# Performance work log

Hardware: AMD Instinct MI355X
Metric: run time of the kernel (lower is better)

The kernel has to match this reference:

```python
import jax, jax.numpy as jnp
import numpy as np

NUM_HEADS = 8

def setup_inputs() -> dict:
    key = jax.random.key(0)
    k1, k2, k3, k4, k5 = jax.random.split(key, 5)
    B, N, C = 4, 2048, 512
    x = jax.random.normal(k1, (B, N, C), dtype=jnp.float32)
    s = 1.0 / np.sqrt(C)
    qkv_w = jax.random.uniform(k2, (3 * C, C), dtype=jnp.float32, minval=-s, maxval=s)
    qkv_b = jax.random.uniform(k3, (3 * C,), dtype=jnp.float32, minval=-s, maxval=s)
    proj_w = jax.random.uniform(k4, (C, C), dtype=jnp.float32, minval=-s, maxval=s)
    proj_b = jax.random.uniform(k5, (C,), dtype=jnp.float32, minval=-s, maxval=s)
    return {"x": x, "qkv_w": qkv_w, "qkv_b": qkv_b, "proj_w": proj_w, "proj_b": proj_b}

def reference(x, qkv_w, qkv_b, proj_w, proj_b):
    B, N, C = x.shape
    H = NUM_HEADS
    D = C // H
    scale = D ** -0.5
    # qkv: [B,N,3C] -> [3,B,H,N,D]
    qkv = (jnp.einsum('bnc,oc->bno', x, qkv_w) + qkv_b)
    qkv = qkv.reshape(B, N, 3, H, D).transpose(2, 0, 3, 1, 4)
    q, k, v = qkv[0], qkv[1], qkv[2]
    attn = jnp.einsum('bhnd,bhmd->bhnm', q, k) * scale  # [B,H,N,N]
    attn = jax.nn.softmax(attn, axis=-1)
    out = jnp.einsum('bhnm,bhmd->bhnd', attn, v)  # [B,H,N,D]
    out = out.transpose(0, 2, 1, 3).reshape(B, N, C)
    return jnp.einsum('bnc,oc->bno', out, proj_w) + proj_b
```

## Files before the change

### kernel.cpp

```cpp
#include <hip/hip_runtime.h>
#include <stdint.h>


typedef short bf16x8 __attribute__((ext_vector_type(8)));
typedef float f32x2  __attribute__((ext_vector_type(2)));
typedef float f32x4  __attribute__((ext_vector_type(4)));
typedef float f32x16 __attribute__((ext_vector_type(16)));
typedef unsigned int u32x4 __attribute__((ext_vector_type(4)));

__device__ __forceinline__ unsigned short f2bf(float f) {
    unsigned int u = __builtin_bit_cast(unsigned int, f);
    u += 0x7fffu + ((u >> 16) & 1u);
    return (unsigned short)(u >> 16);
}
__device__ __forceinline__ unsigned int pk2(float a, float b) {
    return (unsigned int)f2bf(a) | ((unsigned int)f2bf(b) << 16);
}
__device__ __forceinline__ float fexp2(float x) {
    return __builtin_amdgcn_exp2f(x);
}
__device__ __forceinline__ bf16x8 ld8_f32(const float* __restrict__ p) {
    float4 f0 = *(const float4*)p;
    float4 f1 = *(const float4*)(p + 4);
    u32x4 u = {pk2(f0.x, f0.y), pk2(f0.z, f0.w), pk2(f1.x, f1.y), pk2(f1.z, f1.w)};
    return __builtin_bit_cast(bf16x8, u);
}
__device__ __forceinline__ void async16(const void* g, void* l) {
    __builtin_amdgcn_global_load_lds(
        (const __attribute__((address_space(1))) unsigned int*)g,
        (__attribute__((address_space(3))) unsigned int*)l,
        16, 0, 0);
}

#define MFMA16(a, b, c) __builtin_amdgcn_mfma_f32_16x16x32_bf16((a), (b), (c), 0, 0, 0)
#define MFMA32(a, b, c) __builtin_amdgcn_mfma_f32_32x32x16_bf16((a), (b), (c), 0, 0, 0)

__global__ void cvt_bf16(const float* __restrict__ x,
                         const float* __restrict__ w,
                         unsigned short* __restrict__ xb,
                         unsigned short* __restrict__ wb)
{
    const int G = 524288 + 98304;
    for (int idx = blockIdx.x * 256 + threadIdx.x; idx < G; idx += gridDim.x * 256) {
        if (idx < 524288)
            *(bf16x8*)(xb + (size_t)idx * 8) = ld8_f32(x + (size_t)idx * 8);
        else {
            int j = idx - 524288;
            *(bf16x8*)(wb + (size_t)j * 8) = ld8_f32(w + (size_t)j * 8);
        }
    }
}
__global__ void cvt_w2(const float* __restrict__ w, unsigned short* __restrict__ wb)
{
    int idx = blockIdx.x * 256 + threadIdx.x;
    *(bf16x8*)(wb + (size_t)idx * 8) = ld8_f32(w + (size_t)idx * 8);
}

__global__ __launch_bounds__(256, 4)
void gemm_qkv(const unsigned short* __restrict__ A,
              const unsigned short* __restrict__ B,
              const float* __restrict__ bias,
              unsigned short* __restrict__ out0,
              unsigned short* __restrict__ out1,
              unsigned short* __restrict__ out2,
              int K)
{
    __shared__ unsigned short sA[128 * 32];
    __shared__ unsigned short sB[128 * 32];

    const int tid  = threadIdx.x;
    const int wave = tid >> 6, lane = tid & 63;
    const int l = lane & 15, q16 = lane >> 4;
    const int wm = wave >> 1, wn = wave & 1;
    const int bid = blockIdx.x;
    const int slot = bid >> 3;
    const int m0 = ((bid & 7) * 8 + slot / 12) * 128;
    const int n0 = (slot % 12) * 128;

    f32x4 acc[4][4];
#pragma unroll
    for (int i = 0; i < 4; ++i)
#pragma unroll
        for (int j = 0; j < 4; ++j)
            acc[i][j] = (f32x4){0.f, 0.f, 0.f, 0.f};

    for (int k0 = 0; k0 < K; k0 += 32) {
#pragma unroll
        for (int call = 0; call < 2; ++call) {
            int L = call * 256 + tid;
            int r = L >> 2, c = L & 3;
            async16(A + (size_t)(m0 + r) * K + k0 + c * 8, sA + L * 8);
            async16(B + (size_t)(n0 + r) * K + k0 + c * 8, sB + L * 8);
        }
        __syncthreads();

        bf16x8 af[4], bfr[4];
#pragma unroll
        for (int i = 0; i < 4; ++i)
            af[i] = *(const bf16x8*)(sA + ((wm * 64 + i * 16 + l) * 4 + q16) * 8);
#pragma unroll
        for (int j = 0; j < 4; ++j)
            bfr[j] = *(const bf16x8*)(sB + ((wn * 64 + j * 16 + l) * 4 + q16) * 8);
#pragma unroll
        for (int i = 0; i < 4; ++i)
#pragma unroll
            for (int j = 0; j < 4; ++j)
                acc[i][j] = MFMA16(af[i], bfr[j], acc[i][j]);
        __syncthreads();
    }

    const float lscale = 0.18033688f;
#pragma unroll
    for (int i = 0; i < 4; ++i) {
#pragma unroll
        for (int j = 0; j < 4; ++j) {
            int col = n0 + wn * 64 + j * 16 + l;
            float bv = bias[col];
#pragma unroll
            for (int r = 0; r < 4; ++r) {
                int row = m0 + wm * 64 + i * 16 + q16 * 4 + r;
                float val = acc[i][j][r] + bv;
                int which = col >> 9;
                int h = (col >> 6) & 7, d = col & 63;
                int b = row >> 11, n = row & 2047;
                if (which == 0)
                    out0[(size_t)(((b * 8 + h) * 2048) + n) * 64 + d] = f2bf(val * lscale);
                else if (which == 1)
                    out1[(size_t)(((b * 8 + h) * 2048) + n) * 64 + d] = f2bf(val);
                else {
                    int np = (n & ~12) | ((n & 8) >> 1) | ((n & 4) << 1);
                    out2[(size_t)(((b * 8 + h) * 64) + d) * 2048 + np] = f2bf(val);
                }
            }
        }
    }
}

__global__ __launch_bounds__(256, 4)
void gemm_out(const unsigned short* __restrict__ A,
              const unsigned short* __restrict__ B,
              const float* __restrict__ bias,
              float* __restrict__ outf,
              int K, int N)
{
    __shared__ unsigned short sA[64 * 32];
    __shared__ unsigned short sB[128 * 32];

    const int tid  = threadIdx.x;
    const int wave = tid >> 6, lane = tid & 63;
    const int l = lane & 15, q16 = lane >> 4;
    const int wm = wave >> 1, wn = wave & 1;
    const int bid = blockIdx.x;
    const int slot = bid >> 3;
    const int m0 = ((bid & 7) * 16 + (slot >> 2)) * 64;
    const int n0 = (slot & 3) * 128;

    f32x4 acc[2][4];
#pragma unroll
    for (int i = 0; i < 2; ++i)
#pragma unroll
        for (int j = 0; j < 4; ++j)
            acc[i][j] = (f32x4){0.f, 0.f, 0.f, 0.f};

    for (int k0 = 0; k0 < K; k0 += 32) {
        {
            int r = tid >> 2, c = tid & 3;
            async16(A + (size_t)(m0 + r) * K + k0 + c * 8, sA + tid * 8);
        }
#pragma unroll
        for (int call = 0; call < 2; ++call) {
            int L = call * 256 + tid;
            int r = L >> 2, c = L & 3;
            async16(B + (size_t)(n0 + r) * K + k0 + c * 8, sB + L * 8);
        }
        __syncthreads();

        bf16x8 af[2], bfr[4];
#pragma unroll
        for (int i = 0; i < 2; ++i)
            af[i] = *(const bf16x8*)(sA + ((wm * 32 + i * 16 + l) * 4 + q16) * 8);
#pragma unroll
        for (int j = 0; j < 4; ++j)
            bfr[j] = *(const bf16x8*)(sB + ((wn * 64 + j * 16 + l) * 4 + q16) * 8);
#pragma unroll
        for (int i = 0; i < 2; ++i)
#pragma unroll
            for (int j = 0; j < 4; ++j)
                acc[i][j] = MFMA16(af[i], bfr[j], acc[i][j]);
        __syncthreads();
    }

#pragma unroll
    for (int i = 0; i < 2; ++i) {
#pragma unroll
        for (int j = 0; j < 4; ++j) {
            int col = n0 + wn * 64 + j * 16 + l;
            float bv = bias[col];
#pragma unroll
            for (int r = 0; r < 4; ++r) {
                int row = m0 + wm * 32 + i * 16 + q16 * 4 + r;
                outf[(size_t)row * N + col] = acc[i][j][r] + bv;
            }
        }
    }
}

__global__ __launch_bounds__(256, 2)
void attn_fused(const unsigned short* __restrict__ Q,
                const unsigned short* __restrict__ Km,
                const unsigned short* __restrict__ Vt,
                unsigned short* __restrict__ O)
{
    __shared__ unsigned short sK[2][128 * 64];
    __shared__ unsigned short sVt[2][64 * 128];

    const int tid  = threadIdx.x;
    const int wave = tid >> 6, lane = tid & 63;
    const int l31 = lane & 31, h = lane >> 5;
    const int swz = l31 & 7;
    const int bid = blockIdx.x;
    const int slot = bid >> 3;
    const int bh = (bid & 7) * 4 + (slot >> 4);
    const int n0 = (slot & 15) * 128;
    const int q0 = n0 + wave * 32;

    const unsigned short* Kp = Km + (size_t)bh * 2048 * 64;
    const unsigned short* Vp = Vt + (size_t)bh * 64 * 2048;
    const unsigned short* sKf = &sK[0][0];
    const unsigned short* sVf = &sVt[0][0];

    int ka[4], va[2][2];
#pragma unroll
    for (int ks = 0; ks < 4; ++ks)
        ka[ks] = l31 * 64 + ((ks * 2 + h) ^ swz) * 8;
#pragma unroll
    for (int m1 = 0; m1 < 2; ++m1)
#pragma unroll
        for (int ks2 = 0; ks2 < 2; ++ks2)
            va[m1][ks2] = l31 * 128 + ((m1 * 4 + ks2 * 2 + h) ^ swz) * 8;

    int ksrc[4], vsrc[4], dst[4];
#pragma unroll
    for (int c = 0; c < 4; ++c) {
        int s = wave * 256 + c * 64 + lane;
        int rk = s >> 3;
        ksrc[c] = rk * 64 + ((s & 7) ^ (rk & 7)) * 8;
        int rv = s >> 4;
        vsrc[c] = rv * 2048 + ((s & 15) ^ (rv & 7)) * 8;
        dst[c] = s * 8;
    }

    bf16x8 qf[4];
#pragma unroll
    for (int ks = 0; ks < 4; ++ks)
        qf[ks] = *(const bf16x8*)(Q + (size_t)(bh * 2048 + q0 + l31) * 64 + ks * 16 + h * 8);

    f32x16 oacc[2];
#pragma unroll
    for (int dt = 0; dt < 2; ++dt)
#pragma unroll
        for (int e = 0; e < 16; ++e) oacc[dt][e] = 0.f;
    f32x16 Zv;
#pragma unroll
    for (int e = 0; e < 16; ++e) Zv[e] = 0.f;
    f32x2 l2 = {0.f, 0.f};

#pragma unroll
    for (int c = 0; c < 4; ++c) {
        async16(Kp + ksrc[c], (void*)(sKf + dst[c]));
        async16(Vp + vsrc[c], (void*)(sVf + dst[c]));
    }
    __syncthreads();

    for (int it = 0; it < 16; ++it) {
        const int nb = ((it + 1) & 1) * 8192;
        if (it < 15) {
            int kv = (it + 1) * 128;
#pragma unroll
            for (int c = 0; c < 4; ++c)
                async16(Kp + (size_t)kv * 64 + ksrc[c], (void*)(sKf + nb + dst[c]));
        }

        f32x16 sacc[4];
#pragma unroll
        for (int mt = 0; mt < 4; ++mt) {
            bf16x8 kf0 = *(const bf16x8*)(sKf + ka[0] + mt * 2048);
            sacc[mt] = MFMA32(kf0, qf[0], Zv);
#pragma unroll
            for (int ks = 1; ks < 4; ++ks) {
                bf16x8 kf = *(const bf16x8*)(sKf + ka[ks] + mt * 2048);
                sacc[mt] = MFMA32(kf, qf[ks], sacc[mt]);
            }
        }

        if (it < 15) {
            int kv = (it + 1) * 128;
#pragma unroll
            for (int c = 0; c < 4; ++c)
                async16(Vp + (size_t)kv + vsrc[c], (void*)(sVf + nb + dst[c]));
        }

        unsigned int pk[4][4][2];
#pragma unroll
        for (int mt = 0; mt < 4; ++mt)
#pragma unroll
            for (int g = 0; g < 4; ++g) {
                float p0 = fexp2(sacc[mt][4 * g + 0]);
                float p1 = fexp2(sacc[mt][4 * g + 1]);
                float p2 = fexp2(sacc[mt][4 * g + 2]);
                float p3 = fexp2(sacc[mt][4 * g + 3]);
                l2 += (f32x2){p0, p1};
                l2 += (f32x2){p2, p3};
                pk[mt][g][0] = __builtin_amdgcn_perm(
                    __builtin_bit_cast(unsigned int, p1),
                    __builtin_bit_cast(unsigned int, p0), 0x07060302u);
                pk[mt][g][1] = __builtin_amdgcn_perm(
                    __builtin_bit_cast(unsigned int, p3),
                    __builtin_bit_cast(unsigned int, p2), 0x07060302u);
            }

#pragma unroll
        for (int mt = 0; mt < 4; ++mt) {
#pragma unroll
            for (int ks2 = 0; ks2 < 2; ++ks2) {
                u32x4 bu;
                bu[0] = pk[mt][2 * ks2][0];
                bu[1] = pk[mt][2 * ks2][1];
                bu[2] = pk[mt][2 * ks2 + 1][0];
                bu[3] = pk[mt][2 * ks2 + 1][1];
                bf16x8 bfrag = __builtin_bit_cast(bf16x8, bu);
#pragma unroll
                for (int dt = 0; dt < 2; ++dt) {
                    bf16x8 vf = *(const bf16x8*)(sVf + va[mt & 1][ks2]
                                                 + (mt >> 1) * 64 + dt * 4096);
                    oacc[dt] = MFMA32(vf, bfrag, oacc[dt]);
                }
            }
        }

#pragma unroll
        for (int ks = 0; ks < 4; ++ks) ka[ks] ^= 8192;
        va[0][0] ^= 8192; va[0][1] ^= 8192; va[1][0] ^= 8192; va[1][1] ^= 8192;
        __syncthreads();
    }

    float l_run = l2[0] + l2[1];
    l_run += __shfl_xor(l_run, 32);
    const int b = bh >> 3, hh = bh & 7;
    float inv = 1.f / fmaxf(l_run, 1e-20f);
    unsigned short* obase = O + ((size_t)(b * 2048 + q0 + l31)) * 512 + hh * 64;
#pragma unroll
    for (int dt = 0; dt < 2; ++dt)
#pragma unroll
        for (int g = 0; g < 4; ++g) {
            int d = dt * 32 + 8 * g + 4 * h;
            unsigned int w0 = pk2(oacc[dt][4 * g + 0] * inv, oacc[dt][4 * g + 1] * inv);
            unsigned int w1 = pk2(oacc[dt][4 * g + 2] * inv, oacc[dt][4 * g + 3] * inv);
            uint2 w = {w0, w1};
            *(uint2*)(obase + d) = w;
        }
}

extern "C" void kernel_launch(void* const* d_in, const int* in_sizes, int n_in,
                              void* d_out, int out_size, void* d_ws, size_t ws_size,
                              hipStream_t stream)
{
    const float* x      = (const float*)d_in[0];
    const float* qkv_w  = (const float*)d_in[1];
    const float* qkv_b  = (const float*)d_in[2];
    const float* proj_w = (const float*)d_in[3];
    const float* proj_b = (const float*)d_in[4];

    const size_t PER = 4u * 8u * 2048u * 64u;
    unsigned short* q_ws  = (unsigned short*)d_ws;
    unsigned short* k_ws  = q_ws  + PER;
    unsigned short* vt_ws = k_ws  + PER;
    unsigned short* ao_ws = vt_ws + PER;

    unsigned short* xb = (unsigned short*)d_out;
    unsigned short* wb = xb + PER;

    cvt_bf16<<<dim3(640), 256, 0, stream>>>(x, qkv_w, xb, wb);
    gemm_qkv<<<dim3(768), 256, 0, stream>>>(xb, wb, qkv_b, q_ws, k_ws, vt_ws, 512);
    attn_fused<<<dim3(512), 256, 0, stream>>>(q_ws, k_ws, vt_ws, ao_ws);
    cvt_w2<<<dim3(128), 256, 0, stream>>>(proj_w, k_ws);
    gemm_out<<<dim3(512), 256, 0, stream>>>(ao_ws, k_ws, proj_b, (float*)d_out, 512, 512);
}
```

Before: 157.2 us.

## Shrink attention blocks to two waves and drop K/V double buffering

Each attention block now has 128 threads and covers 64 queries instead of 256 threads and 128 queries, and the grid doubles to 1024 blocks. The K/V shared tiles are single-buffered: the whole next tile is loaded after a barrier at the end of each iteration, rather than prefetched into a second buffer during compute. This halves LDS per block so more blocks can be resident per CU, but each tile load is no longer overlapped with compute inside the block. Each K/V tile is also reused by fewer queries, which raises global/L2 traffic per query.

Measured after the change: 160.5 us. +2.1%, slower.

```diff
diff --git a/kernel.cpp b/kernel.cpp
--- a/kernel.cpp
+++ b/kernel.cpp
@@ -205,14 +205,14 @@
     }
 }
 
-__global__ __launch_bounds__(256, 2)
+__global__ __launch_bounds__(128, 2)
 void attn_fused(const unsigned short* __restrict__ Q,
                 const unsigned short* __restrict__ Km,
                 const unsigned short* __restrict__ Vt,
                 unsigned short* __restrict__ O)
 {
-    __shared__ unsigned short sK[2][128 * 64];
-    __shared__ unsigned short sVt[2][64 * 128];
+    __shared__ unsigned short sK[128 * 64];
+    __shared__ unsigned short sVt[64 * 128];
 
     const int tid  = threadIdx.x;
     const int wave = tid >> 6, lane = tid & 63;
@@ -220,14 +220,12 @@
     const int swz = l31 & 7;
     const int bid = blockIdx.x;
     const int slot = bid >> 3;
-    const int bh = (bid & 7) * 4 + (slot >> 4);
-    const int n0 = (slot & 15) * 128;
+    const int bh = (bid & 7) * 4 + (slot >> 5);
+    const int n0 = (slot & 31) * 64;
     const int q0 = n0 + wave * 32;
 
     const unsigned short* Kp = Km + (size_t)bh * 2048 * 64;
     const unsigned short* Vp = Vt + (size_t)bh * 64 * 2048;
-    const unsigned short* sKf = &sK[0][0];
-    const unsigned short* sVf = &sVt[0][0];
 
     int ka[4], va[2][2];
 #pragma unroll
@@ -239,10 +237,10 @@
         for (int ks2 = 0; ks2 < 2; ++ks2)
             va[m1][ks2] = l31 * 128 + ((m1 * 4 + ks2 * 2 + h) ^ swz) * 8;
 
-    int ksrc[4], vsrc[4], dst[4];
-#pragma unroll
-    for (int c = 0; c < 4; ++c) {
-        int s = wave * 256 + c * 64 + lane;
+    int ksrc[8], vsrc[8], dst[8];
+#pragma unroll
+    for (int c = 0; c < 8; ++c) {
+        int s = c * 128 + tid;
         int rk = s >> 3;
         ksrc[c] = rk * 64 + ((s & 7) ^ (rk & 7)) * 8;
         int rv = s >> 4;
@@ -266,38 +264,24 @@
     f32x2 l2 = {0.f, 0.f};
 
 #pragma unroll
-    for (int c = 0; c < 4; ++c) {
-        async16(Kp + ksrc[c], (void*)(sKf + dst[c]));
-        async16(Vp + vsrc[c], (void*)(sVf + dst[c]));
-    }
-    __syncthreads();
+    for (int c = 0; c < 8; ++c) {
+        async16(Kp + ksrc[c], (void*)(&sK[0] + dst[c]));
+        async16(Vp + vsrc[c], (void*)(&sVt[0] + dst[c]));
+    }
 
     for (int it = 0; it < 16; ++it) {
-        const int nb = ((it + 1) & 1) * 8192;
-        if (it < 15) {
-            int kv = (it + 1) * 128;
-#pragma unroll
-            for (int c = 0; c < 4; ++c)
-                async16(Kp + (size_t)kv * 64 + ksrc[c], (void*)(sKf + nb + dst[c]));
-        }
+        __syncthreads();
 
         f32x16 sacc[4];
 #pragma unroll
         for (int mt = 0; mt < 4; ++mt) {
-            bf16x8 kf0 = *(const bf16x8*)(sKf + ka[0] + mt * 2048);
+            bf16x8 kf0 = *(const bf16x8*)(&sK[0] + ka[0] + mt * 2048);
             sacc[mt] = MFMA32(kf0, qf[0], Zv);
 #pragma unroll
             for (int ks = 1; ks < 4; ++ks) {
-                bf16x8 kf = *(const bf16x8*)(sKf + ka[ks] + mt * 2048);
+                bf16x8 kf = *(const bf16x8*)(&sK[0] + ka[ks] + mt * 2048);
                 sacc[mt] = MFMA32(kf, qf[ks], sacc[mt]);
             }
-        }
-
-        if (it < 15) {
-            int kv = (it + 1) * 128;
-#pragma unroll
-            for (int c = 0; c < 4; ++c)
-                async16(Vp + (size_t)kv + vsrc[c], (void*)(sVf + nb + dst[c]));
         }
 
         unsigned int pk[4][4][2];
@@ -331,17 +315,22 @@
                 bf16x8 bfrag = __builtin_bit_cast(bf16x8, bu);
 #pragma unroll
                 for (int dt = 0; dt < 2; ++dt) {
-                    bf16x8 vf = *(const bf16x8*)(sVf + va[mt & 1][ks2]
+                    bf16x8 vf = *(const bf16x8*)(&sVt[0] + va[mt & 1][ks2]
                                                  + (mt >> 1) * 64 + dt * 4096);
                     oacc[dt] = MFMA32(vf, bfrag, oacc[dt]);
                 }
             }
         }
 
-#pragma unroll
-        for (int ks = 0; ks < 4; ++ks) ka[ks] ^= 8192;
-        va[0][0] ^= 8192; va[0][1] ^= 8192; va[1][0] ^= 8192; va[1][1] ^= 8192;
-        __syncthreads();
+        __syncthreads();
+        if (it < 15) {
+            int kv = (it + 1) * 128;
+#pragma unroll
+            for (int c = 0; c < 8; ++c) {
+                async16(Kp + (size_t)kv * 64 + ksrc[c], (void*)(&sK[0] + dst[c]));
+                async16(Vp + (size_t)kv + vsrc[c], (void*)(&sVt[0] + dst[c]));
+            }
+        }
     }
 
     float l_run = l2[0] + l2[1];
@@ -382,7 +371,7 @@
 
     cvt_bf16<<<dim3(640), 256, 0, stream>>>(x, qkv_w, xb, wb);
     gemm_qkv<<<dim3(768), 256, 0, stream>>>(xb, wb, qkv_b, q_ws, k_ws, vt_ws, 512);
-    attn_fused<<<dim3(512), 256, 0, stream>>>(q_ws, k_ws, vt_ws, ao_ws);
+    attn_fused<<<dim3(1024), 128, 0, stream>>>(q_ws, k_ws, vt_ws, ao_ws);
     cvt_w2<<<dim3(128), 256, 0, stream>>>(proj_w, k_ws);
     gemm_out<<<dim3(512), 256, 0, stream>>>(ao_ws, k_ws, proj_b, (float*)d_out, 512, 512);
 }
```

## Load GEMM fragments directly from global memory with register double-buffering

Applied to the files above, without the earlier changes.

Both projection GEMMs drop the LDS staging and __syncthreads. Each wave now loads its MFMA operand fragments straight from global memory into registers, with a two-stage prefetch (k and k+32) that overlaps the loads with MFMA work. Occupancy for gemm_qkv is lowered to 3 blocks to make room for the extra registers. The trade-off is that operands are no longer shared through LDS, so every wave re-reads its own A/B rows and the kernels lean more on L2/L1 bandwidth.

New measurement: 196.5 us. 25.0% more time.

```diff
diff --git a/kernel.cpp b/kernel.cpp
--- a/kernel.cpp
+++ b/kernel.cpp
@@ -56,7 +56,7 @@
     *(bf16x8*)(wb + (size_t)idx * 8) = ld8_f32(w + (size_t)idx * 8);
 }
 
-__global__ __launch_bounds__(256, 4)
+__global__ __launch_bounds__(256, 3)
 void gemm_qkv(const unsigned short* __restrict__ A,
               const unsigned short* __restrict__ B,
               const float* __restrict__ bias,
@@ -65,9 +65,6 @@
               unsigned short* __restrict__ out2,
               int K)
 {
-    __shared__ unsigned short sA[128 * 32];
-    __shared__ unsigned short sB[128 * 32];
-
     const int tid  = threadIdx.x;
     const int wave = tid >> 6, lane = tid & 63;
     const int l = lane & 15, q16 = lane >> 4;
@@ -77,6 +74,10 @@
     const int m0 = ((bid & 7) * 8 + slot / 12) * 128;
     const int n0 = (slot % 12) * 128;
 
+    const unsigned short* Ap = A + (size_t)(m0 + wm * 64 + l) * K + q16 * 8;
+    const unsigned short* Bp = B + (size_t)(n0 + wn * 64 + l) * K + q16 * 8;
+    const size_t rstep = (size_t)16 * K;
+
     f32x4 acc[4][4];
 #pragma unroll
     for (int i = 0; i < 4; ++i)
@@ -84,29 +85,35 @@
         for (int j = 0; j < 4; ++j)
             acc[i][j] = (f32x4){0.f, 0.f, 0.f, 0.f};
 
-    for (int k0 = 0; k0 < K; k0 += 32) {
-#pragma unroll
-        for (int call = 0; call < 2; ++call) {
-            int L = call * 256 + tid;
-            int r = L >> 2, c = L & 3;
-            async16(A + (size_t)(m0 + r) * K + k0 + c * 8, sA + L * 8);
-            async16(B + (size_t)(n0 + r) * K + k0 + c * 8, sB + L * 8);
-        }
-        __syncthreads();
-
-        bf16x8 af[4], bfr[4];
+    bf16x8 a0[4], b0[4], a1[4], b1[4];
+#pragma unroll
+    for (int i = 0; i < 4; ++i) {
+        a0[i] = *(const bf16x8*)(Ap + i * rstep);
+        b0[i] = *(const bf16x8*)(Bp + i * rstep);
+    }
+    for (int k0 = 0; k0 < K; k0 += 64) {
+#pragma unroll
+        for (int i = 0; i < 4; ++i) {
+            a1[i] = *(const bf16x8*)(Ap + i * rstep + k0 + 32);
+            b1[i] = *(const bf16x8*)(Bp + i * rstep + k0 + 32);
+        }
 #pragma unroll
         for (int i = 0; i < 4; ++i)
-            af[i] = *(const bf16x8*)(sA + ((wm * 64 + i * 16 + l) * 4 + q16) * 8);
-#pragma unroll
-        for (int j = 0; j < 4; ++j)
-            bfr[j] = *(const bf16x8*)(sB + ((wn * 64 + j * 16 + l) * 4 + q16) * 8);
+#pragma unroll
+            for (int j = 0; j < 4; ++j)
+                acc[i][j] = MFMA16(a0[i], b0[j], acc[i][j]);
+        if (k0 + 64 < K) {
+#pragma unroll
+            for (int i = 0; i < 4; ++i) {
+                a0[i] = *(const bf16x8*)(Ap + i * rstep + k0 + 64);
+                b0[i] = *(const bf16x8*)(Bp + i * rstep + k0 + 64);
+            }
+        }
 #pragma unroll
         for (int i = 0; i < 4; ++i)
 #pragma unroll
             for (int j = 0; j < 4; ++j)
-                acc[i][j] = MFMA16(af[i], bfr[j], acc[i][j]);
-        __syncthreads();
+                acc[i][j] = MFMA16(a1[i], b1[j], acc[i][j]);
     }
 
     const float lscale = 0.18033688f;
@@ -143,9 +150,6 @@
               float* __restrict__ outf,
               int K, int N)
 {
-    __shared__ unsigned short sA[64 * 32];
-    __shared__ unsigned short sB[128 * 32];
-
     const int tid  = threadIdx.x;
     const int wave = tid >> 6, lane = tid & 63;
     const int l = lane & 15, q16 = lane >> 4;
@@ -155,6 +159,10 @@
     const int m0 = ((bid & 7) * 16 + (slot >> 2)) * 64;
     const int n0 = (slot & 3) * 128;
 
+    const unsigned short* Ap = A + (size_t)(m0 + wm * 32 + l) * K + q16 * 8;
+    const unsigned short* Bp = B + (size_t)(n0 + wn * 64 + l) * K + q16 * 8;
+    const size_t rstep = (size_t)16 * K;
+
     f32x4 acc[2][4];
 #pragma unroll
     for (int i = 0; i < 2; ++i)
@@ -162,32 +170,33 @@
         for (int j = 0; j < 4; ++j)
             acc[i][j] = (f32x4){0.f, 0.f, 0.f, 0.f};
 
-    for (int k0 = 0; k0 < K; k0 += 32) {
-        {
-            int r = tid >> 2, c = tid & 3;
-            async16(A + (size_t)(m0 + r) * K + k0 + c * 8, sA + tid * 8);
-        }
-#pragma unroll
-        for (int call = 0; call < 2; ++call) {
-            int L = call * 256 + tid;
-            int r = L >> 2, c = L & 3;
-            async16(B + (size_t)(n0 + r) * K + k0 + c * 8, sB + L * 8);
-        }
-        __syncthreads();
-
-        bf16x8 af[2], bfr[4];
+    bf16x8 a0[2], b0[4], a1[2], b1[4];
+#pragma unroll
+    for (int i = 0; i < 2; ++i) a0[i] = *(const bf16x8*)(Ap + i * rstep);
+#pragma unroll
+    for (int j = 0; j < 4; ++j) b0[j] = *(const bf16x8*)(Bp + j * rstep);
+
+    for (int k0 = 0; k0 < K; k0 += 64) {
+#pragma unroll
+        for (int i = 0; i < 2; ++i) a1[i] = *(const bf16x8*)(Ap + i * rstep + k0 + 32);
+#pragma unroll
+        for (int j = 0; j < 4; ++j) b1[j] = *(const bf16x8*)(Bp + j * rstep + k0 + 32);
 #pragma unroll
         for (int i = 0; i < 2; ++i)
-            af[i] = *(const bf16x8*)(sA + ((wm * 32 + i * 16 + l) * 4 + q16) * 8);
-#pragma unroll
-        for (int j = 0; j < 4; ++j)
-            bfr[j] = *(const bf16x8*)(sB + ((wn * 64 + j * 16 + l) * 4 + q16) * 8);
+#pragma unroll
+            for (int j = 0; j < 4; ++j)
+                acc[i][j] = MFMA16(a0[i], b0[j], acc[i][j]);
+        if (k0 + 64 < K) {
+#pragma unroll
+            for (int i = 0; i < 2; ++i) a0[i] = *(const bf16x8*)(Ap + i * rstep + k0 + 64);
+#pragma unroll
+            for (int j = 0; j < 4; ++j) b0[j] = *(const bf16x8*)(Bp + j * rstep + k0 + 64);
+        }
 #pragma unroll
         for (int i = 0; i < 2; ++i)
 #pragma unroll
             for (int j = 0; j < 4; ++j)
-                acc[i][j] = MFMA16(af[i], bfr[j], acc[i][j]);
-        __syncthreads();
+                acc[i][j] = MFMA16(a1[i], b1[j], acc[i][j]);
     }
 
 #pragma unroll
```
